# Performance work log

Measured on AMD Instinct MI355X. Metric: run time of the kernel, lower is better.

## Reference

```python
import jax, jax.numpy as jnp
import numpy as np

B, S, DIN, DIM, H = 2, 2304, 1024, 1024, 16
HEAD_DIM = DIM // H            # 64
ROT_DIM = HEAD_DIM             # partial_rotary_factor = 1
BASE = 10000.0
EPS = 1e-6


def setup_inputs() -> dict:
    key = jax.random.key(0)
    ks = jax.random.split(key, 6)
    return {
        "input": jax.random.normal(ks[0], (B, S, DIN), dtype=jnp.float32),
        "qkv_w": jax.random.normal(ks[1], (3 * DIM, DIN), dtype=jnp.float32) * 0.02,
        "qkv_b": jnp.zeros((3 * DIM,), dtype=jnp.float32),
        "q_scale": jnp.ones((DIM,), dtype=jnp.float32),
        "k_scale": jnp.ones((DIM,), dtype=jnp.float32),
        "proj_w": jax.random.normal(ks[2], (DIN, DIM), dtype=jnp.float32) * 0.02,
        "proj_b": jnp.zeros((DIN,), dtype=jnp.float32),
        "height": 48,
        "width": 48,
    }


def _rms_norm(x, scale):
    # RMSNorm over the full inner dim (QKNorm), learned scale
    var = jnp.mean(x * x, axis=-1, keepdims=True)
    return x * jax.lax.rsqrt(var + EPS) * scale


def _rope_1d(x, pos):
    # x: (b, n, h, d_ax), pos: (n,) float; rotate_half-style RoPE
    d = x.shape[-1]
    inv_freq = 1.0 / (BASE ** (jnp.arange(0, d, 2, dtype=jnp.float32) / d))  # (d/2,)
    ang = pos[:, None] * inv_freq                                            # (n, d/2)
    cos = jnp.concatenate([jnp.cos(ang), jnp.cos(ang)], axis=-1)[None, :, None, :]
    sin = jnp.concatenate([jnp.sin(ang), jnp.sin(ang)], axis=-1)[None, :, None, :]
    x1, x2 = jnp.split(x, 2, axis=-1)
    rot = jnp.concatenate([-x2, x1], axis=-1)
    return x * cos + rot * sin


def _rope_2d(x, height, width):
    # axial 2D RoPE: first half of rotary dims keyed by row, second half by col
    n = height * width
    idx = jnp.arange(n, dtype=jnp.float32)
    rows = jnp.floor(idx / width)
    cols = jnp.mod(idx, width)
    half = ROT_DIM // 2
    x_r = _rope_1d(x[..., :half], rows)
    x_c = _rope_1d(x[..., half:ROT_DIM], cols)
    return jnp.concatenate([x_r, x_c, x[..., ROT_DIM:]], axis=-1)


def reference(input, qkv_w, qkv_b, q_scale, k_scale, proj_w, proj_b, height, width):
    b, n, _ = input.shape
    qkv = input @ qkv_w.T + qkv_b                       # (b, n, 3*dim)
    q, k, v = jnp.split(qkv, 3, axis=-1)
    q = _rms_norm(q, q_scale)
    k = _rms_norm(k, k_scale)
    # (b, n, h, d)
    q = q.reshape(b, n, H, HEAD_DIM)
    k = k.reshape(b, n, H, HEAD_DIM)
    v = v.reshape(b, n, H, HEAD_DIM)
    q = _rope_2d(q, height, width)
    k = _rope_2d(k, height, width)
    scale = HEAD_DIM ** (-0.5)
    # (b, h, q, k)
    scores = jnp.einsum("bqhd,bkhd->bhqk", q, k) * scale
    attn = jax.nn.softmax(scores, axis=-1)
    out = jnp.einsum("bhqk,bkhd->bqhd", attn, v)        # (b, n, h, d)
    out = out.reshape(b, n, DIM)
    return out @ proj_w.T + proj_b
```

## Files before the change

### kernel.cpp

```cpp
#include <hip/hip_runtime.h>
#include <math.h>

#define BB   2
#define SS   2304
#define DINC 1024
#define DIMC 1024
#define HH   16
#define HD   64

typedef _Float16 half_t;
typedef __attribute__((ext_vector_type(4))) _Float16 half4;
typedef __attribute__((ext_vector_type(8))) _Float16 half8;
typedef __attribute__((ext_vector_type(4))) float    f32x4;

#define LOG2E 1.44269504088896340736f
#define EXP2(x) __builtin_amdgcn_exp2f(x)

__device__ __forceinline__ half4 lo4(half8 x) { return (half4){x[0], x[1], x[2], x[3]}; }
__device__ __forceinline__ half4 hi4(half8 x) { return (half4){x[4], x[5], x[6], x[7]}; }

#define GLOAD_LDS16(gp, lp)                                                     \
    __builtin_amdgcn_global_load_lds(                                           \
        (const __attribute__((address_space(1))) void*)(gp),                    \
        (__attribute__((address_space(3))) void*)(lp), 16, 0, 0)

template<int RB>
__global__ __launch_bounds__(256)
void convert_tile_f16(const float* __restrict__ src, half_t* __restrict__ dst, int K)
{
    constexpr int EPT = RB * 32 / 256;
    const int mb = blockIdx.x;
    const int kb = blockIdx.y;
    const int t  = threadIdx.x;
    const int e0 = t * EPT;
    const int mm = e0 >> 5;
    const int kk = e0 & 31;
    const float* sp = src + (size_t)(mb * RB + mm) * K + kb * 32 + kk;
    half_t*      dp = dst + ((size_t)mb * (K >> 5) + kb) * (RB * 32) + mm * 32 + kk;
    #pragma unroll
    for (int g = 0; g < EPT / 4; ++g) {
        float4 v = *(const float4*)(sp + 4 * g);
        dp[4 * g + 0] = (half_t)v.x; dp[4 * g + 1] = (half_t)v.y;
        dp[4 * g + 2] = (half_t)v.z; dp[4 * g + 3] = (half_t)v.w;
    }
}

template<int BN, bool OUT_HALF>
__global__ __launch_bounds__(256)
void gemm_mfma(const half_t* __restrict__ Ah, const half_t* __restrict__ Bh,
               const float* __restrict__ bias, void* __restrict__ Cout,
               int M, int N, int K)
{
    constexpr int MT = (BN == 128) ? 4 : 2;
    constexpr int NT = 4;
    const int KB = K >> 5;
    __shared__ half_t As[8192];
    __shared__ half_t Bs[2 * BN * 32];

    const int t    = threadIdx.x;
    const int w    = t >> 6;
    const int lane = t & 63;
    const int l15  = lane & 15, quad = lane >> 4;
    const int wr   = (BN == 128) ? (w >> 1) : w;
    const int wc   = (BN == 128) ? (w & 1) : 0;
    const int mb   = blockIdx.y, nb = blockIdx.x;

    f32x4 acc[MT][NT];
    #pragma unroll
    for (int mt = 0; mt < MT; ++mt)
        #pragma unroll
        for (int nt = 0; nt < NT; ++nt) acc[mt][nt] = (f32x4){0.f, 0.f, 0.f, 0.f};

    const half_t* atile = Ah + (size_t)mb * KB * 4096;
    const half_t* btile = Bh + (size_t)nb * KB * (BN * 32);

    for (int kb = 0; kb < KB; kb += 2) {
        #pragma unroll
        for (int u = 0; u < 2; ++u) {
            const half_t* at = atile + (size_t)(kb + u) * 4096;
            const half_t* bt = btile + (size_t)(kb + u) * (BN * 32);
            #pragma unroll
            for (int v = 0; v < 2; ++v) {
                const int ch = w * 2 + v;
                GLOAD_LDS16(at + ch * 512 + lane * 8, As + u * 4096 + ch * 512);
            }
            if (BN == 128) {
                #pragma unroll
                for (int v = 0; v < 2; ++v) {
                    const int ch = w * 2 + v;
                    GLOAD_LDS16(bt + ch * 512 + lane * 8, Bs + u * 4096 + ch * 512);
                }
            } else {
                GLOAD_LDS16(bt + w * 512 + lane * 8, Bs + u * (BN * 32) + w * 512);
            }
        }
        __syncthreads();

        #pragma unroll
        for (int u = 0; u < 2; ++u) {
            half8 af[MT], bf[NT];
            #pragma unroll
            for (int mt = 0; mt < MT; ++mt)
                af[mt] = *(const half8*)(As + u * 4096
                                         + (wr * (MT * 16) + mt * 16 + l15) * 32 + quad * 8);
            #pragma unroll
            for (int nt = 0; nt < NT; ++nt)
                bf[nt] = *(const half8*)(Bs + u * (BN * 32)
                                         + (wc * 64 + nt * 16 + l15) * 32 + quad * 8);
            #pragma unroll
            for (int mt = 0; mt < MT; ++mt)
                #pragma unroll
                for (int nt = 0; nt < NT; ++nt)
                    acc[mt][nt] = __builtin_amdgcn_mfma_f32_16x16x32_f16(
                        af[mt], bf[nt], acc[mt][nt], 0, 0, 0);
        }
        __syncthreads();
    }

    const int bm = mb * 128, bn = nb * BN;
    #pragma unroll
    for (int nt = 0; nt < NT; ++nt) {
        const int n  = bn + wc * 64 + nt * 16 + l15;
        const float bv = bias[n];
        #pragma unroll
        for (int mt = 0; mt < MT; ++mt) {
            const int m0 = bm + wr * (MT * 16) + mt * 16 + quad * 4;
            #pragma unroll
            for (int rg = 0; rg < 4; ++rg) {
                const float v = acc[mt][nt][rg] + bv;
                if (OUT_HALF) ((half_t*)Cout)[(size_t)(m0 + rg) * N + n] = (half_t)v;
                else          ((float*) Cout)[(size_t)(m0 + rg) * N + n] = v;
            }
        }
    }
}

__global__ __launch_bounds__(256)
void normrope_v6(half_t* __restrict__ qkvh, const float* __restrict__ q_scale,
                 const float* __restrict__ k_scale, const int* __restrict__ wptr,
                 half_t* __restrict__ Kf, half_t* __restrict__ Vf)
{
    const int token = blockIdx.x;
    const int s     = token % SS;
    const int b     = token / SS;
    const int w     = *wptr;
    const int t     = threadIdx.x;
    const float rowp = (float)(s / w);
    const float colp = (float)(s % w);

    half_t* base = qkvh + (size_t)token * 3072;

    const int fr = s >> 5;
    const int jt = (s >> 4) & 1;

    {
        half4 v4 = *(const half4*)(base + 2048 + 4 * t);
        const int dabs0 = 4 * t;
        const int h  = dabs0 >> 6;
        const int vq = (s & 15) >> 2;
        const int vi = s & 3;
        half_t* vdst = Vf + ((size_t)(b * HH + h) * 72 + fr) * 2048 + jt * 1024;
        #pragma unroll
        for (int ii = 0; ii < 4; ++ii) {
            const int d   = (dabs0 + ii) & 63;
            const int dt  = d >> 4;
            vdst[(size_t)(dt >> 1) * 512 + ((d & 15) + 16 * vq) * 8 + (dt & 1) * 4 + vi]
                = v4[ii];
        }
    }

    __shared__ float buf[DIMC];
    __shared__ float red[4];

    const int km = s & 15;

    #pragma unroll
    for (int sel = 0; sel < 2; ++sel) {
        half_t* row = base + sel * DIMC;
        const float* scp = sel ? k_scale : q_scale;

        half4 xh = *(const half4*)(row + 4 * t);
        float x0 = (float)xh[0], x1 = (float)xh[1], x2 = (float)xh[2], x3 = (float)xh[3];
        float ss = x0 * x0 + x1 * x1 + x2 * x2 + x3 * x3;
        #pragma unroll
        for (int o = 32; o >= 1; o >>= 1) ss += __shfl_xor(ss, o);
        if ((t & 63) == 0) red[t >> 6] = ss;
        __syncthreads();

        const float rinv = rsqrtf((red[0] + red[1] + red[2] + red[3]) * (1.0f / DIMC) + 1e-6f);
        float4 g = *(const float4*)(scp + 4 * t);
        buf[4 * t + 0] = x0 * rinv * g.x;
        buf[4 * t + 1] = x1 * rinv * g.y;
        buf[4 * t + 2] = x2 * rinv * g.z;
        buf[4 * t + 3] = x3 * rinv * g.w;
        __syncthreads();

        const float qsc = sel ? 1.0f : (0.125f * LOG2E);

        #pragma unroll
        for (int pp = 0; pp < 2; ++pp) {
            const int p = t + pp * 256;
            const int h = p >> 5;
            const int r = p & 31;
            const int j = r & 15;
            const float pos = (r < 16) ? rowp : colp;
            const int d1 = (r < 16) ? j : (32 + j);
            const int d2 = d1 + 16;
            const float freq = exp2f((float)j * -0.83048202372f);
            const float ang  = pos * freq;
            float sn, cs;
            __sincosf(ang, &sn, &cs);
            const float a1 = buf[h * HD + d1], a2 = buf[h * HD + d2];
            const float o1 = (a1 * cs - a2 * sn) * qsc;
            const float o2 = (a2 * cs + a1 * sn) * qsc;
            if (sel == 0) {
                row[h * HD + d1] = (half_t)o1;
                row[h * HD + d2] = (half_t)o2;
            } else {
                half_t* kdst = Kf + ((size_t)(b * HH + h) * 72 + fr) * 2048 + jt * 1024;
                kdst[(size_t)(d1 >> 5) * 512 + (km + 16 * ((d1 & 31) >> 3)) * 8 + (d1 & 7)]
                    = (half_t)o1;
                kdst[(size_t)(d2 >> 5) * 512 + (km + 16 * ((d2 & 31) >> 3)) * 8 + (d2 & 7)]
                    = (half_t)o2;
            }
        }
        __syncthreads();
    }
}

__global__ __launch_bounds__(256, 4)
void flash_attn_mfma5(const half_t* __restrict__ qkvh, const half_t* __restrict__ Kf,
                      const half_t* __restrict__ Vf, half_t* __restrict__ attn_h)
{
    const int flat = blockIdx.x;
    const int xcd  = flat & 7;
    const int jj   = flat >> 3;
    const int bh   = xcd * 4 + (jj / 36);
    const int qtb  = jj % 36;
    const int b    = bh >> 4, h = bh & 15;
    const int t    = threadIdx.x;
    const int w    = t >> 6;
    const int jt   = w & 1;
    const int qh   = w >> 1;
    const int lane = t & 63;
    const int l15  = lane & 15, quad = lane >> 4;

    const size_t tb = (size_t)b * SS;
    const int q0 = qtb * 64;

    __shared__ half_t KV[2][4096];
    __shared__ float  mlb[4][32][2];

    half8 qf[2][2];
    #pragma unroll
    for (int qt = 0; qt < 2; ++qt)
        #pragma unroll
        for (int dt2 = 0; dt2 < 2; ++dt2)
            qf[qt][dt2] = *(const half8*)(qkvh + (tb + q0 + qh * 32 + qt * 16 + l15) * 3072
                                          + h * HD + dt2 * 32 + quad * 8);

    f32x4 acc[4][2];
    float m_i[2], l_i[2];
    #pragma unroll
    for (int qt = 0; qt < 2; ++qt) {
        m_i[qt] = -INFINITY; l_i[qt] = 0.f;
        #pragma unroll
        for (int dt = 0; dt < 4; ++dt) acc[dt][qt] = (f32x4){0.f, 0.f, 0.f, 0.f};
    }

    const half_t* kbase = Kf + (size_t)bh * 72 * 2048;
    const half_t* vbase = Vf + (size_t)bh * 72 * 2048;

    GLOAD_LDS16(kbase + w * 512 + lane * 8, &KV[0][0]    + w * 512);
    GLOAD_LDS16(vbase + w * 512 + lane * 8, &KV[0][2048] + w * 512);

    for (int fr = 0; fr < 72; ++fr) {
        const int cur = fr & 1;
        __syncthreads();
        if (fr + 1 < 72) {
            const half_t* kg = kbase + (size_t)(fr + 1) * 2048;
            const half_t* vg = vbase + (size_t)(fr + 1) * 2048;
            GLOAD_LDS16(kg + w * 512 + lane * 8, &KV[cur ^ 1][0]    + w * 512);
            GLOAD_LDS16(vg + w * 512 + lane * 8, &KV[cur ^ 1][2048] + w * 512);
        }

        const half_t* kb = &KV[cur][jt * 1024];
        half8 kf0 = *(const half8*)(kb + lane * 8);
        half8 kf1 = *(const half8*)(kb + 512 + lane * 8);
        const half_t* vb = &KV[cur][2048 + jt * 1024];
        half8 v01 = *(const half8*)(vb + lane * 8);
        half8 v23 = *(const half8*)(vb + 512 + lane * 8);
        half4 vf[4] = {lo4(v01), hi4(v01), lo4(v23), hi4(v23)};

        f32x4 sc[2];
        #pragma unroll
        for (int qt = 0; qt < 2; ++qt) {
            sc[qt] = (f32x4){0.f, 0.f, 0.f, 0.f};
            sc[qt] = __builtin_amdgcn_mfma_f32_16x16x32_f16(kf0, qf[qt][0], sc[qt], 0, 0, 0);
            sc[qt] = __builtin_amdgcn_mfma_f32_16x16x32_f16(kf1, qf[qt][1], sc[qt], 0, 0, 0);
        }

        half4 pf[2];
        #pragma unroll
        for (int qt = 0; qt < 2; ++qt) {
            float mx = fmaxf(fmaxf(sc[qt][0], sc[qt][1]), fmaxf(sc[qt][2], sc[qt][3]));
            mx = fmaxf(mx, __shfl_xor(mx, 16));
            mx = fmaxf(mx, __shfl_xor(mx, 32));
            if (__any(mx > m_i[qt])) {
                const float mn = fmaxf(m_i[qt], mx);
                const float alpha = EXP2(m_i[qt] - mn);
                m_i[qt] = mn;
                l_i[qt] *= alpha;
                #pragma unroll
                for (int dt = 0; dt < 4; ++dt) acc[dt][qt] *= alpha;
            }
            const float m = m_i[qt];
            const float p0 = EXP2(sc[qt][0] - m);
            const float p1 = EXP2(sc[qt][1] - m);
            const float p2 = EXP2(sc[qt][2] - m);
            const float p3 = EXP2(sc[qt][3] - m);
            l_i[qt] += (p0 + p1) + (p2 + p3);
            pf[qt] = (half4){(half_t)p0, (half_t)p1, (half_t)p2, (half_t)p3};
        }

        #pragma unroll
        for (int dt = 0; dt < 4; ++dt)
            #pragma unroll
            for (int qt = 0; qt < 2; ++qt)
                acc[dt][qt] = __builtin_amdgcn_mfma_f32_16x16x16f16(
                    vf[dt], pf[qt], acc[dt][qt], 0, 0, 0);
    }

    #pragma unroll
    for (int qt = 0; qt < 2; ++qt) {
        float lq = l_i[qt];
        lq += __shfl_xor(lq, 16);
        lq += __shfl_xor(lq, 32);
        if (quad == 0) {
            mlb[w][qt * 16 + l15][0] = m_i[qt];
            mlb[w][qt * 16 + l15][1] = lq;
        }
    }
    __syncthreads();

    float fac[2];
    #pragma unroll
    for (int qt = 0; qt < 2; ++qt) {
        const int q = qt * 16 + l15;
        const float m0 = mlb[qh * 2 + 0][q][0], m1 = mlb[qh * 2 + 1][q][0];
        const float M  = fmaxf(m0, m1);
        const float L  = mlb[qh * 2 + 0][q][1] * EXP2(m0 - M)
                       + mlb[qh * 2 + 1][q][1] * EXP2(m1 - M);
        fac[qt] = EXP2(m_i[qt] - M) / L;
    }

    float* Ob = (float*)KV;
    #pragma unroll
    for (int ph = 0; ph < 2; ++ph) {
        if (jt == ph) {
            #pragma unroll
            for (int dt = 0; dt < 4; ++dt)
                #pragma unroll
                for (int qt = 0; qt < 2; ++qt)
                    #pragma unroll
                    for (int rg = 0; rg < 4; ++rg) {
                        const int d = dt * 16 + quad * 4 + rg;
                        const int q = qt * 16 + l15;
                        const float v = acc[dt][qt][rg] * fac[qt];
                        if (ph == 0) Ob[qh * 2048 + d * 32 + q] = v;
                        else         Ob[qh * 2048 + d * 32 + q] += v;
                    }
        }
        __syncthreads();
    }

    {
        const int q   = t >> 2;
        const int ds  = (t & 3) * 16;
        const int qh2 = q >> 5, qq = q & 31;
        const size_t mrow = tb + q0 + q;
        const int mb2 = (int)(mrow >> 7);
        const int mm  = (int)(mrow & 127);
        #pragma unroll
        for (int g = 0; g < 4; ++g) {
            const int dd = ds + 4 * g;
            const int kb2 = (h * HD + dd) >> 5;
            const int kk  = dd & 31;
            half4 o;
            o[0] = (half_t)Ob[qh2 * 2048 + (dd + 0) * 32 + qq];
            o[1] = (half_t)Ob[qh2 * 2048 + (dd + 1) * 32 + qq];
            o[2] = (half_t)Ob[qh2 * 2048 + (dd + 2) * 32 + qq];
            o[3] = (half_t)Ob[qh2 * 2048 + (dd + 3) * 32 + qq];
            *(half4*)(attn_h + ((size_t)mb2 * 32 + kb2) * 4096 + mm * 32 + kk) = o;
        }
    }
}

extern "C" void kernel_launch(void* const* d_in, const int* in_sizes, int n_in,
                              void* d_out, int out_size, void* d_ws, size_t ws_size,
                              hipStream_t stream)
{
    const float* input   = (const float*)d_in[0];
    const float* qkv_w   = (const float*)d_in[1];
    const float* qkv_b   = (const float*)d_in[2];
    const float* q_scale = (const float*)d_in[3];
    const float* k_scale = (const float*)d_in[4];
    const float* proj_w  = (const float*)d_in[5];
    const float* proj_b  = (const float*)d_in[6];
    const int*   width   = (const int*)d_in[8];
    float* out = (float*)d_out;

    half_t* qkvh   = (half_t*)d_ws;
    half_t* attn_h = qkvh   + (size_t)4608 * 3072;
    half_t* Vf     = attn_h + (size_t)4608 * 1024;
    half_t* Ah     = Vf     + (size_t)32 * 72 * 2048;
    half_t* Bh1    = Ah     + (size_t)4608 * 1024;
    half_t* Bh2    = Bh1    + (size_t)3072 * 1024;
    half_t* Kf     = Ah;

    const int M = BB * SS;

    convert_tile_f16<128><<<dim3(M / 128, DINC / 32),        256, 0, stream>>>(input,  Ah,  DINC);
    convert_tile_f16<128><<<dim3(3 * DIMC / 128, DINC / 32), 256, 0, stream>>>(qkv_w, Bh1, DINC);
    convert_tile_f16<64><<<dim3(DINC / 64, DIMC / 32),       256, 0, stream>>>(proj_w, Bh2, DIMC);

    gemm_mfma<128, true><<<dim3(3 * DIMC / 128, M / 128), 256, 0, stream>>>(
        Ah, Bh1, qkv_b, qkvh, M, 3 * DIMC, DINC);

    normrope_v6<<<M, 256, 0, stream>>>(qkvh, q_scale, k_scale, width, Kf, Vf);

    flash_attn_mfma5<<<dim3(SS / 64 * BB * HH), 256, 0, stream>>>(qkvh, Kf, Vf, attn_h);

    gemm_mfma<64, false><<<dim3(DINC / 64, M / 128), 256, 0, stream>>>(
        attn_h, Bh2, proj_b, out, M, DINC, DIMC);
}
```

Baseline: 275.1 us.

## Load K/V fragments directly into registers with two-deep prefetch instead of LDS

The flash attention kernel no longer stages K/V tiles through double-buffered shared memory with global_load_lds and per-tile __syncthreads. Each wave now loads its own pre-swizzled K/V fragments straight from global memory into registers, prefetching one tile ahead in a manually unrolled two-tile loop. This removes the per-iteration block barrier and the LDS round trip. The cost is more global/L2 traffic, since waves sharing a jt half both fetch the same data, and higher register pressure. The output staging buffer is padded to 33 columns to reduce LDS bank conflicts.

```diff
diff --git a/kernel.cpp b/kernel.cpp
--- a/kernel.cpp
+++ b/kernel.cpp
@@ -229,7 +229,7 @@
 }
 
 __global__ __launch_bounds__(256, 4)
-void flash_attn_mfma5(const half_t* __restrict__ qkvh, const half_t* __restrict__ Kf,
+void flash_attn_mfma6(const half_t* __restrict__ qkvh, const half_t* __restrict__ Kf,
                       const half_t* __restrict__ Vf, half_t* __restrict__ attn_h)
 {
     const int flat = blockIdx.x;
@@ -248,8 +248,8 @@
     const size_t tb = (size_t)b * SS;
     const int q0 = qtb * 64;
 
-    __shared__ half_t KV[2][4096];
-    __shared__ float  mlb[4][32][2];
+    __shared__ float mlb[4][32][2];
+    __shared__ float Ob[2][64][33];
 
     half8 qf[2][2];
     #pragma unroll
@@ -268,30 +268,11 @@
         for (int dt = 0; dt < 4; ++dt) acc[dt][qt] = (f32x4){0.f, 0.f, 0.f, 0.f};
     }
 
-    const half_t* kbase = Kf + (size_t)bh * 72 * 2048;
-    const half_t* vbase = Vf + (size_t)bh * 72 * 2048;
-
-    GLOAD_LDS16(kbase + w * 512 + lane * 8, &KV[0][0]    + w * 512);
-    GLOAD_LDS16(vbase + w * 512 + lane * 8, &KV[0][2048] + w * 512);
-
-    for (int fr = 0; fr < 72; ++fr) {
-        const int cur = fr & 1;
-        __syncthreads();
-        if (fr + 1 < 72) {
-            const half_t* kg = kbase + (size_t)(fr + 1) * 2048;
-            const half_t* vg = vbase + (size_t)(fr + 1) * 2048;
-            GLOAD_LDS16(kg + w * 512 + lane * 8, &KV[cur ^ 1][0]    + w * 512);
-            GLOAD_LDS16(vg + w * 512 + lane * 8, &KV[cur ^ 1][2048] + w * 512);
-        }
-
-        const half_t* kb = &KV[cur][jt * 1024];
-        half8 kf0 = *(const half8*)(kb + lane * 8);
-        half8 kf1 = *(const half8*)(kb + 512 + lane * 8);
-        const half_t* vb = &KV[cur][2048 + jt * 1024];
-        half8 v01 = *(const half8*)(vb + lane * 8);
-        half8 v23 = *(const half8*)(vb + 512 + lane * 8);
+    const half_t* kpl = Kf + (size_t)bh * 72 * 2048 + jt * 1024 + lane * 8;
+    const half_t* vpl = Vf + (size_t)bh * 72 * 2048 + jt * 1024 + lane * 8;
+
+    auto step = [&](half8 kf0, half8 kf1, half8 v01, half8 v23) {
         half4 vf[4] = {lo4(v01), hi4(v01), lo4(v23), hi4(v23)};
-
         f32x4 sc[2];
         #pragma unroll
         for (int qt = 0; qt < 2; ++qt) {
@@ -299,7 +280,6 @@
             sc[qt] = __builtin_amdgcn_mfma_f32_16x16x32_f16(kf0, qf[qt][0], sc[qt], 0, 0, 0);
             sc[qt] = __builtin_amdgcn_mfma_f32_16x16x32_f16(kf1, qf[qt][1], sc[qt], 0, 0, 0);
         }
-
         half4 pf[2];
         #pragma unroll
         for (int qt = 0; qt < 2; ++qt) {
@@ -322,13 +302,40 @@
             l_i[qt] += (p0 + p1) + (p2 + p3);
             pf[qt] = (half4){(half_t)p0, (half_t)p1, (half_t)p2, (half_t)p3};
         }
-
         #pragma unroll
         for (int dt = 0; dt < 4; ++dt)
             #pragma unroll
             for (int qt = 0; qt < 2; ++qt)
                 acc[dt][qt] = __builtin_amdgcn_mfma_f32_16x16x16f16(
                     vf[dt], pf[qt], acc[dt][qt], 0, 0, 0);
+    };
+
+    half8 kA0 = *(const half8*)(kpl);
+    half8 kA1 = *(const half8*)(kpl + 512);
+    half8 vA0 = *(const half8*)(vpl);
+    half8 vA1 = *(const half8*)(vpl + 512);
+
+    for (int fr2 = 0; fr2 < 36; ++fr2) {
+        const int fr = fr2 * 2;
+        const half_t* kB = kpl + (size_t)(fr + 1) * 2048;
+        const half_t* vB = vpl + (size_t)(fr + 1) * 2048;
+        half8 kB0 = *(const half8*)(kB);
+        half8 kB1 = *(const half8*)(kB + 512);
+        half8 vB0 = *(const half8*)(vB);
+        half8 vB1 = *(const half8*)(vB + 512);
+
+        step(kA0, kA1, vA0, vA1);
+
+        if (fr + 2 < 72) {
+            const half_t* kA = kpl + (size_t)(fr + 2) * 2048;
+            const half_t* vA = vpl + (size_t)(fr + 2) * 2048;
+            kA0 = *(const half8*)(kA);
+            kA1 = *(const half8*)(kA + 512);
+            vA0 = *(const half8*)(vA);
+            vA1 = *(const half8*)(vA + 512);
+        }
+
+        step(kB0, kB1, vB0, vB1);
     }
 
     #pragma unroll
@@ -354,7 +361,6 @@
         fac[qt] = EXP2(m_i[qt] - M) / L;
     }
 
-    float* Ob = (float*)KV;
     #pragma unroll
     for (int ph = 0; ph < 2; ++ph) {
         if (jt == ph) {
@@ -367,8 +373,8 @@
                         const int d = dt * 16 + quad * 4 + rg;
                         const int q = qt * 16 + l15;
                         const float v = acc[dt][qt][rg] * fac[qt];
-                        if (ph == 0) Ob[qh * 2048 + d * 32 + q] = v;
-                        else         Ob[qh * 2048 + d * 32 + q] += v;
+                        if (ph == 0) Ob[qh][d][q] = v;
+                        else         Ob[qh][d][q] += v;
                     }
         }
         __syncthreads();
@@ -387,10 +393,10 @@
             const int kb2 = (h * HD + dd) >> 5;
             const int kk  = dd & 31;
             half4 o;
-            o[0] = (half_t)Ob[qh2 * 2048 + (dd + 0) * 32 + qq];
-            o[1] = (half_t)Ob[qh2 * 2048 + (dd + 1) * 32 + qq];
-            o[2] = (half_t)Ob[qh2 * 2048 + (dd + 2) * 32 + qq];
-            o[3] = (half_t)Ob[qh2 * 2048 + (dd + 3) * 32 + qq];
+            o[0] = (half_t)Ob[qh2][dd + 0][qq];
+            o[1] = (half_t)Ob[qh2][dd + 1][qq];
+            o[2] = (half_t)Ob[qh2][dd + 2][qq];
+            o[3] = (half_t)Ob[qh2][dd + 3][qq];
             *(half4*)(attn_h + ((size_t)mb2 * 32 + kb2) * 4096 + mm * 32 + kk) = o;
         }
     }
@@ -429,7 +435,7 @@
 
     normrope_v6<<<M, 256, 0, stream>>>(qkvh, q_scale, k_scale, width, Kf, Vf);
 
-    flash_attn_mfma5<<<dim3(SS / 64 * BB * HH), 256, 0, stream>>>(qkvh, Kf, Vf, attn_h);
+    flash_attn_mfma6<<<dim3(SS / 64 * BB * HH), 256, 0, stream>>>(qkvh, Kf, Vf, attn_h);
 
     gemm_mfma<64, false><<<dim3(DINC / 64, M / 128), 256, 0, stream>>>(
         attn_h, Bh2, proj_b, out, M, DINC, DIMC);
```

Measured after the change: 271.0 us. Within noise of the previous version (-1.5%).
